# Performance work log

Measured on AMD Instinct MI355X. Metric: run time of the kernel, lower is better.

The kernel has to match this reference:

```python
import jax, jax.numpy as jnp
import numpy as np

IN_CH = 512
HID_CH = 512
NUM_HEADS = HID_CH // 32  # 16 heads, 32 channels each
GN_GROUPS = 32
EPS = 1e-6


def group_norm(x, scale, bias):
    # x: (b, c, t); GroupNorm over (channels-in-group, t)
    b, c, t = x.shape
    xg = x.reshape(b, GN_GROUPS, c // GN_GROUPS, t)
    mean = xg.mean(axis=(2, 3), keepdims=True)
    var = xg.var(axis=(2, 3), keepdims=True)
    xg = (xg - mean) * jax.lax.rsqrt(var + EPS)
    return xg.reshape(b, c, t) * scale[None, :, None] + bias[None, :, None]


def setup_inputs() -> dict:
    key = jax.random.key(0)
    ks = jax.random.split(key, 12)
    b, t = 16, 8192
    s = 0.02
    return {
        "x": jax.random.normal(ks[0], (b, IN_CH, t), dtype=jnp.float32),
        "gn_scale": jnp.ones((IN_CH,), jnp.float32),
        "gn_bias": jnp.zeros((IN_CH,), jnp.float32),
        "wq": jax.random.normal(ks[1], (HID_CH, IN_CH), jnp.float32) * s,
        "bq": jnp.zeros((HID_CH,), jnp.float32),
        "wk": jax.random.normal(ks[2], (HID_CH, IN_CH), jnp.float32) * s,
        "bk": jnp.zeros((HID_CH,), jnp.float32),
        "wv": jax.random.normal(ks[3], (HID_CH, IN_CH), jnp.float32) * s,
        "bv": jnp.zeros((HID_CH,), jnp.float32),
        "wp": jax.random.normal(ks[4], (IN_CH, HID_CH), jnp.float32) * s,
        "bp": jnp.zeros((IN_CH,), jnp.float32),
    }


def reference(x, gn_scale, gn_bias, wq, bq, wk, bk, wv, bv, wp, bp):
    b, _, t = x.shape
    n = NUM_HEADS
    hc = HID_CH // n  # 32 channels per head
    h = group_norm(x, gn_scale, gn_bias)
    # 1x1 conv == channel GEMM: (b,c_in,t) -> (b,c_out,t)
    q = jnp.einsum('oc,bct->bot', wq, h) + bq[None, :, None]
    k = jnp.einsum('oc,bct->bot', wk, h) + bk[None, :, None]
    v = jnp.einsum('oc,bct->bot', wv, h) + bv[None, :, None]
    q = q.reshape(b, n, hc, t)
    k = k.reshape(b, n, hc, t)
    v = v.reshape(b, n, hc, t)
    # q: softmax over channel dim; k: rearranged to (.., t, c), softmax over c
    q = jax.nn.softmax(q, axis=2)          # (b,n,c,t), softmax over c
    k = jax.nn.softmax(k, axis=2)          # softmax over c (dim=-1 after b n t c rearrange)
    w = jnp.einsum('bnct,bndt->bncd', q, k)   # (b,n,c,c) small cxc matrix
    h = jnp.einsum('bncd,bndt->bnct', w, v)   # (b,n,c,t)
    h = h.reshape(b, HID_CH, t)
    out = jnp.einsum('oc,bct->bot', wp, h) + bp[None, :, None]
    return x + out
```

## Files before the change

### kernel.cpp

```cpp
#include <hip/hip_runtime.h>

typedef _Float16 f16;
typedef _Float16 f16x8 __attribute__((ext_vector_type(8)));
typedef _Float16 f16x4 __attribute__((ext_vector_type(4)));
typedef float f32x4 __attribute__((ext_vector_type(4)));
typedef float f32x16 __attribute__((ext_vector_type(16)));


__device__ __forceinline__ void gl_lds16(const f16* g, const void* lds) {
    __builtin_amdgcn_global_load_lds((const __attribute__((address_space(1))) void*)g,
                                     (__attribute__((address_space(3))) void*)lds, 16, 0, 0);
}

__global__ __launch_bounds__(256) void k_tr(const float* __restrict__ x, f16* __restrict__ xT,
                                            float* __restrict__ part,
                                            const float* __restrict__ wv, f16* __restrict__ WvT) {
    int tid = threadIdx.x;
    if (blockIdx.x >= 16384) {
        int idx = (blockIdx.x - 16384) * 256 + tid;
        int c = idx >> 9, e = idx & 511;
        WvT[idx] = (f16)wv[(size_t)e * 512 + c];
        return;
    }
    __shared__ f16 ldsT[64][72];
    int tt = blockIdx.x & 127, ct = (blockIdx.x >> 7) & 7, b = blockIdx.x >> 10;
    int cc = tid >> 2, tq = tid & 3;
    int c = ct * 64 + cc;
    const float* xp = x + ((size_t)b * 512 + c) * 8192 + tt * 64 + tq * 16;
    float s = 0.f, s2 = 0.f;
#pragma unroll
    for (int q4 = 0; q4 < 4; ++q4) {
        f32x4 v = *(const f32x4*)(xp + q4 * 4);
#pragma unroll
        for (int j = 0; j < 4; ++j) {
            ldsT[tq * 16 + q4 * 4 + j][cc] = (f16)v[j];
            s += v[j]; s2 += v[j] * v[j];
        }
    }
#pragma unroll
    for (int k = 1; k < 64; k <<= 1) { s += __shfl_xor(s, k); s2 += __shfl_xor(s2, k); }
    if ((tid & 63) == 0) {
        float* pp = part + (((size_t)b * 32 + ct * 4 + (tid >> 6)) * 128 + tt) * 2;
        pp[0] = s; pp[1] = s2;
    }
    __syncthreads();
    int tl = tid >> 2, cq = tid & 3;
    f16x8 v0 = *(const f16x8*)(&ldsT[tl][cq * 16]);
    f16x8 v1 = *(const f16x8*)(&ldsT[tl][cq * 16 + 8]);
    f16* hp = xT + ((size_t)b * 8192 + tt * 64 + tl) * 512 + ct * 64 + cq * 16;
    *(f16x8*)(hp) = v0;
    *(f16x8*)(hp + 8) = v1;
}

__global__ __launch_bounds__(256) void k_prep(const float* __restrict__ wq, const float* __restrict__ wk,
                                              const float* __restrict__ wv,
                                              const float* __restrict__ gsc, const float* __restrict__ gbi,
                                              const float* __restrict__ part,
                                              const float* __restrict__ bq, const float* __restrict__ bk,
                                              f16* __restrict__ Wqkp2, float* __restrict__ qkb,
                                              float* __restrict__ u, float* __restrict__ stats) {
    __shared__ float scn[512], bi[512], red[256];
    int tid = threadIdx.x;
    int blk = blockIdx.x;
    int b = (blk < 256) ? (blk >> 4) : ((blk - 256) >> 3);
    {
        int g = tid >> 3, ch = tid & 7;
        const float* pp = part + (((size_t)b * 32 + g) * 128 + ch * 16) * 2;
        float s = 0.f, s2 = 0.f;
        for (int t2 = 0; t2 < 16; ++t2) { s += pp[t2 * 2]; s2 += pp[t2 * 2 + 1]; }
        scn[tid] = s; bi[tid] = s2;
    }
    __syncthreads();
    if (tid < 32) {
        float S = 0.f, S2 = 0.f;
#pragma unroll
        for (int j = 0; j < 8; ++j) { S += scn[tid * 8 + j]; S2 += bi[tid * 8 + j]; }
        float mean = S * (1.f / 131072.f);
        float var  = S2 * (1.f / 131072.f) - mean * mean;
        float rstd = rsqrtf(var + 1e-6f);
        red[tid] = mean;
        red[128 + tid] = rstd;
        if (blk >= 256 && ((blk - 256) & 7) == 0) {
            stats[(b * 32 + tid) * 2 + 0] = mean;
            stats[(b * 32 + tid) * 2 + 1] = rstd;
        }
    }
    __syncthreads();
    for (int i = tid; i < 512; i += 256) {
        float sc = gsc[i] * red[128 + (i >> 4)];
        scn[i] = sc;
        bi[i] = gbi[i] - red[i >> 4] * sc;
    }
    __syncthreads();
    if (blk < 256) {
        int rg = blk & 15;
        int pr = rg * 64 + (tid >> 2);
        int cq = tid & 3;
        int hg = pr >> 8, ri = pr & 255;
        int hl = ri >> 6, qk = (ri >> 5) & 1, ch = ri & 31;
        int src = (hg * 4 + hl) * 32 + ch;
        const float* wrow = (qk ? wk : wq) + (size_t)src * 512;
        f16* orow = Wqkp2 + ((size_t)b * 1024 + pr) * 512;
        float dot = 0.f;
        for (int c0 = cq * 128; c0 < cq * 128 + 128; c0 += 8) {
            f16x8 o8;
#pragma unroll
            for (int j = 0; j < 8; ++j) {
                float wv_ = wrow[c0 + j] * scn[c0 + j];
                o8[j] = (f16)wv_;
                dot += wv_ * bi[c0 + j];
            }
            *(f16x8*)(orow + c0) = o8;
        }
        red[tid] = dot;
        __syncthreads();
        if (cq == 0)
            qkb[(size_t)b * 1024 + pr] = red[tid] + red[tid + 1] + red[tid + 2] + red[tid + 3]
                                         + (qk ? bk[src] : bq[src]);
    } else {
        int ug = (blk - 256) & 7;
        int e = ug * 64 + (tid >> 2);
        int cq = tid & 3;
        const float* wrow = wv + (size_t)e * 512;
        float dot = 0.f;
        for (int c = cq * 128; c < cq * 128 + 128; ++c) dot += wrow[c] * bi[c];
        red[tid] = dot;
        __syncthreads();
        if (cq == 0) u[(size_t)b * 512 + e] = red[tid] + red[tid + 1] + red[tid + 2] + red[tid + 3];
    }
}

__device__ __forceinline__ void gemm_core(const f16* __restrict__ Abase, int lda,
                                          const f16* __restrict__ Bbase,
                                          char* smem, int tid, f32x4 acc[4][4]) {
    const int lane = tid & 63, wave = tid >> 6;
    const int wm = wave >> 1, wn = wave & 1;
    char* As = smem;
    char* Bs = smem + 16384;
    const int srow = (lane >> 3);
    const int schunk = (lane & 7) ^ srow;
    for (int kt = 0; kt < 8; ++kt) {
#pragma unroll
        for (int i = 0; i < 4; ++i) {
            int row = (wave * 4 + i) * 8 + srow;
            gl_lds16(Abase + (size_t)row * lda + kt * 64 + schunk * 8, As + (wave * 4 + i) * 1024);
            gl_lds16(Bbase + (size_t)row * 512 + kt * 64 + schunk * 8, Bs + (wave * 4 + i) * 1024);
        }
        __syncthreads();
#pragma unroll
        for (int ks = 0; ks < 2; ++ks) {
            f16x8 af[4], bf[4];
#pragma unroll
            for (int i = 0; i < 4; ++i) {
                int row = wm * 64 + i * 16 + (lane & 15);
                int ch = (ks * 4 + (lane >> 4)) ^ (lane & 7);
                af[i] = *(const f16x8*)(As + row * 128 + ch * 16);
            }
#pragma unroll
            for (int j = 0; j < 4; ++j) {
                int row = wn * 64 + j * 16 + (lane & 15);
                int ch = (ks * 4 + (lane >> 4)) ^ (lane & 7);
                bf[j] = *(const f16x8*)(Bs + row * 128 + ch * 16);
            }
#pragma unroll
            for (int i = 0; i < 4; ++i)
#pragma unroll
                for (int j = 0; j < 4; ++j)
                    acc[i][j] = __builtin_amdgcn_mfma_f32_16x16x32_f16(af[i], bf[j], acc[i][j], 0, 0, 0);
        }
        __syncthreads();
    }
}

__global__ __launch_bounds__(256, 2) void k_qk_w(const f16* __restrict__ xT, const f16* __restrict__ Wqkp2,
                                                 const float* __restrict__ qkb, f16* __restrict__ w_part) {
    __shared__ __align__(16) char smem[49152];
    int tid = threadIdx.x, lane = tid & 63, wave = tid >> 6;
    int bid = blockIdx.x;
    int lb = (bid & 7) * 512 + (bid >> 3);
    int batch = lb >> 8;
    int rem = lb & 255;
    int tt = rem >> 2, hg = rem & 3;
    const f16* Abase = Wqkp2 + ((size_t)batch * 1024 + hg * 256) * 512;
    const f16* Bbase = xT + ((size_t)batch * 8192 + (size_t)tt * 128) * 512;
    char* As = smem;
    char* Bs = smem + 32768;
    const int srow = lane >> 3;
    const int schunk = (lane & 7) ^ srow;
    f32x4 acc[4][8];
#pragma unroll
    for (int i = 0; i < 4; ++i)
#pragma unroll
        for (int j = 0; j < 8; ++j) acc[i][j] = (f32x4){0.f, 0.f, 0.f, 0.f};

    for (int kt = 0; kt < 8; ++kt) {
#pragma unroll
        for (int i = 0; i < 8; ++i) {
            int g = wave * 8 + i;
            gl_lds16(Abase + (size_t)(g * 8 + srow) * 512 + kt * 64 + schunk * 8, As + g * 1024);
        }
#pragma unroll
        for (int i = 0; i < 4; ++i) {
            int g = wave * 4 + i;
            gl_lds16(Bbase + (size_t)(g * 8 + srow) * 512 + kt * 64 + schunk * 8, Bs + g * 1024);
        }
        __syncthreads();
#pragma unroll
        for (int ks = 0; ks < 2; ++ks) {
            f16x8 af[4];
#pragma unroll
            for (int i = 0; i < 4; ++i) {
                int row = wave * 64 + i * 16 + (lane & 15);
                int ch = (ks * 4 + (lane >> 4)) ^ (lane & 7);
                af[i] = *(const f16x8*)(As + row * 128 + ch * 16);
            }
#pragma unroll
            for (int j = 0; j < 8; ++j) {
                int row = j * 16 + (lane & 15);
                int ch = (ks * 4 + (lane >> 4)) ^ (lane & 7);
                f16x8 bf = *(const f16x8*)(Bs + row * 128 + ch * 16);
#pragma unroll
                for (int i = 0; i < 4; ++i)
                    acc[i][j] = __builtin_amdgcn_mfma_f32_16x16x32_f16(af[i], bf, acc[i][j], 0, 0, 0);
            }
        }
        __syncthreads();
    }

    float qb[2][8];
#pragma unroll
    for (int qk = 0; qk < 2; ++qk)
#pragma unroll
        for (int i2 = 0; i2 < 2; ++i2)
#pragma unroll
            for (int r = 0; r < 4; ++r)
                qb[qk][i2 * 4 + r] = qkb[(size_t)batch * 1024 + hg * 256 + wave * 64 + qk * 32 +
                                         i2 * 16 + (lane >> 4) * 4 + r];
    f16* qbuf = (f16*)(smem + wave * 9216);
    f16* kbuf = qbuf + 32 * 72;
    f32x16 wacc;
#pragma unroll
    for (int i = 0; i < 16; ++i) wacc[i] = 0.f;

#pragma unroll
    for (int th = 0; th < 2; ++th) {
#pragma unroll
        for (int jl = 0; jl < 4; ++jl) {
            int j = th * 4 + jl;
#pragma unroll
            for (int qk = 0; qk < 2; ++qk) {
                int ib = qk * 2;
                float v0[8];
#pragma unroll
                for (int i2 = 0; i2 < 2; ++i2)
#pragma unroll
                    for (int r = 0; r < 4; ++r)
                        v0[i2 * 4 + r] = acc[ib + i2][j][r] + qb[qk][i2 * 4 + r];
                float mx = v0[0];
#pragma unroll
                for (int i = 1; i < 8; ++i) mx = fmaxf(mx, v0[i]);
                mx = fmaxf(mx, __shfl_xor(mx, 16));
                mx = fmaxf(mx, __shfl_xor(mx, 32));
                float s = 0.f;
#pragma unroll
                for (int i = 0; i < 8; ++i) { v0[i] = __expf(v0[i] - mx); s += v0[i]; }
                s += __shfl_xor(s, 16);
                s += __shfl_xor(s, 32);
                float inv = 1.f / s;
                f16* dst = qk ? kbuf : qbuf;
                int tcol = jl * 16 + (lane & 15);
#pragma unroll
                for (int i2 = 0; i2 < 2; ++i2)
#pragma unroll
                    for (int r = 0; r < 4; ++r) {
                        int c = i2 * 16 + (lane >> 4) * 4 + r;
                        dst[c * 72 + tcol] = (f16)(v0[i2 * 4 + r] * inv);
                    }
            }
        }
#pragma unroll
        for (int ks = 0; ks < 4; ++ks) {
            f16x8 a  = *(const f16x8*)(qbuf + (lane & 31) * 72 + ks * 16 + (lane >> 5) * 8);
            f16x8 bb = *(const f16x8*)(kbuf + (lane & 31) * 72 + ks * 16 + (lane >> 5) * 8);
            wacc = __builtin_amdgcn_mfma_f32_32x32x16_f16(a, bb, wacc, 0, 0, 0);
        }
    }
    int ghead = hg * 4 + wave;
    f16* wpo = w_part + (((size_t)tt * 16 + batch) * 16 + ghead) * 1024;
#pragma unroll
    for (int r = 0; r < 16; ++r) {
        int row = (r & 3) + 8 * (r >> 2) + 4 * (lane >> 5);
        wpo[row * 32 + (lane & 31)] = (f16)wacc[r];
    }
}

__global__ __launch_bounds__(256) void k_wreduce(const f16* __restrict__ w_part, float* __restrict__ w_red) {
    int blk = blockIdx.x;
    int tid = threadIdx.x;
    f32x4 s = (f32x4){0.f, 0.f, 0.f, 0.f};
    for (int tt = 0; tt < 64; ++tt) {
        f16x4 v = *(const f16x4*)(w_part + ((size_t)tt * 256 + blk) * 1024 + tid * 4);
#pragma unroll
        for (int j = 0; j < 4; ++j) s[j] += (float)v[j];
    }
    *(f32x4*)(w_red + (size_t)blk * 1024 + tid * 4) = s;
}

__global__ __launch_bounds__(256) void k_wpe(const float* __restrict__ w_red, const float* __restrict__ wp,
                                             const float* __restrict__ bv, const float* __restrict__ u,
                                             const float* __restrict__ bp,
                                             f16* __restrict__ wpe, float* __restrict__ bias_p) {
    __shared__ float wl[16384];
    __shared__ float bred[256];
    int tid = threadIdx.x;
    int b = blockIdx.x >> 3, ot = blockIdx.x & 7;
    for (int idx = tid; idx < 16384; idx += 256) wl[idx] = w_red[(size_t)b * 16384 + idx];
    __syncthreads();
    int o = ot * 64 + (tid >> 2);
    int cq = tid & 3;
    float bacc = 0.f;
#pragma unroll
    for (int ng = 0; ng < 4; ++ng) {
        int n = cq * 4 + ng;
        float a[32];
#pragma unroll
        for (int d = 0; d < 32; ++d) a[d] = 0.f;
        for (int e = 0; e < 32; ++e) {
            float wv = wp[(size_t)o * 512 + n * 32 + e];
#pragma unroll
            for (int d = 0; d < 32; ++d) a[d] += wv * wl[n * 1024 + e * 32 + d];
        }
#pragma unroll
        for (int dc = 0; dc < 4; ++dc) {
            f16x8 o8;
#pragma unroll
            for (int j = 0; j < 8; ++j) o8[j] = (f16)a[dc * 8 + j];
            *(f16x8*)(wpe + ((size_t)b * 512 + o) * 512 + n * 32 + dc * 8) = o8;
        }
#pragma unroll
        for (int d = 0; d < 32; ++d) bacc += a[d] * (bv[n * 32 + d] + u[(size_t)b * 512 + n * 32 + d]);
    }
    bred[tid] = bacc;
    __syncthreads();
    if ((tid & 3) == 0)
        bias_p[(size_t)b * 512 + o] = bp[o] + bred[tid] + bred[tid + 1] + bred[tid + 2] + bred[tid + 3];
}

__global__ __launch_bounds__(256) void k_wfin(const f16* __restrict__ wpe, const f16* __restrict__ WvT,
                                              const float* __restrict__ gsc, const float* __restrict__ stats,
                                              f16* __restrict__ Wfin) {
    __shared__ __align__(16) char smem[34816];
    int tid = threadIdx.x, lane = tid & 63, wave = tid >> 6;
    int wm = wave >> 1, wn = wave & 1;
    int bid = blockIdx.x;
    int b = bid >> 4, mt = (bid >> 2) & 3, nt = bid & 3;
    const f16* Abase = wpe + (size_t)b * 262144 + (size_t)mt * 128 * 512;
    const f16* Bbase = WvT + (size_t)nt * 128 * 512;
    f32x4 acc[4][4];
#pragma unroll
    for (int i = 0; i < 4; ++i)
#pragma unroll
        for (int j = 0; j < 4; ++j) acc[i][j] = (f32x4){0.f, 0.f, 0.f, 0.f};
    gemm_core(Abase, 512, Bbase, smem, tid, acc);
    float scnj[4];
#pragma unroll
    for (int j = 0; j < 4; ++j) {
        int col = nt * 128 + wn * 64 + j * 16 + (lane & 15);
        scnj[j] = gsc[col] * stats[(b * 32 + (col >> 4)) * 2 + 1];
    }
    f16* epi = (f16*)smem;
#pragma unroll
    for (int i = 0; i < 4; ++i)
#pragma unroll
        for (int j = 0; j < 4; ++j)
#pragma unroll
            for (int r = 0; r < 4; ++r) {
                int m = wm * 64 + i * 16 + (lane >> 4) * 4 + r;
                int n = wn * 64 + j * 16 + (lane & 15);
                epi[m * 136 + n] = (f16)(acc[i][j][r] * scnj[j]);
            }
    __syncthreads();
#pragma unroll
    for (int rr = 0; rr < 8; ++rr) {
        int row = wave * 32 + (lane >> 4) * 8 + rr;
        f16x8 vv = *(const f16x8*)(epi + row * 136 + (lane & 15) * 8);
        *(f16x8*)(Wfin + (size_t)b * 262144 + (size_t)(mt * 128 + row) * 512 + nt * 128 + (lane & 15) * 8) = vv;
    }
}

__global__ __launch_bounds__(256, 2) void k_out(const f16* __restrict__ xT, const f16* __restrict__ Wfin,
                                                const float* __restrict__ x, const float* __restrict__ bias_p,
                                                float* __restrict__ out) {
    __shared__ __align__(16) char smem[49152];
    int tid = threadIdx.x, lane = tid & 63, wave = tid >> 6;
    int bid = blockIdx.x;
    int lb = (bid & 7) * 256 + (bid >> 3);
    int batch = lb >> 7;
    int rem = lb & 127;
    int tt = rem >> 1, ot2 = rem & 1;
    const f16* Abase = Wfin + (size_t)batch * 262144 + (size_t)ot2 * 256 * 512;
    const f16* Bbase = xT + ((size_t)batch * 8192 + (size_t)tt * 128) * 512;
    char* As = smem;
    char* Bs = smem + 32768;
    const int srow = lane >> 3;
    const int schunk = (lane & 7) ^ srow;
    f32x4 acc[4][8];
#pragma unroll
    for (int i = 0; i < 4; ++i)
#pragma unroll
        for (int j = 0; j < 8; ++j) acc[i][j] = (f32x4){0.f, 0.f, 0.f, 0.f};

    for (int kt = 0; kt < 8; ++kt) {
#pragma unroll
        for (int i = 0; i < 8; ++i) {
            int g = wave * 8 + i;
            gl_lds16(Abase + (size_t)(g * 8 + srow) * 512 + kt * 64 + schunk * 8, As + g * 1024);
        }
#pragma unroll
        for (int i = 0; i < 4; ++i) {
            int g = wave * 4 + i;
            gl_lds16(Bbase + (size_t)(g * 8 + srow) * 512 + kt * 64 + schunk * 8, Bs + g * 1024);
        }
        __syncthreads();
#pragma unroll
        for (int ks = 0; ks < 2; ++ks) {
            f16x8 af[4];
#pragma unroll
            for (int i = 0; i < 4; ++i) {
                int row = wave * 64 + i * 16 + (lane & 15);
                int ch = (ks * 4 + (lane >> 4)) ^ (lane & 7);
                af[i] = *(const f16x8*)(As + row * 128 + ch * 16);
            }
#pragma unroll
            for (int j = 0; j < 8; ++j) {
                int row = j * 16 + (lane & 15);
                int ch = (ks * 4 + (lane >> 4)) ^ (lane & 7);
                f16x8 bf = *(const f16x8*)(Bs + row * 128 + ch * 16);
#pragma unroll
                for (int i = 0; i < 4; ++i)
                    acc[i][j] = __builtin_amdgcn_mfma_f32_16x16x32_f16(af[i], bf, acc[i][j], 0, 0, 0);
            }
        }
        __syncthreads();
    }

    f16* ep = (f16*)smem;
    const int orow_in = (lane >> 4) * 4;
    for (int pp = 0; pp < 2; ++pp) {
        __syncthreads();
        if ((wave >> 1) == pp) {
            f16* myep = ep + (size_t)(wave & 1) * 64 * 132;
#pragma unroll
            for (int i = 0; i < 4; ++i)
#pragma unroll
                for (int j = 0; j < 8; ++j)
#pragma unroll
                    for (int r = 0; r < 4; ++r)
                        myep[(i * 16 + orow_in + r) * 132 + j * 16 + (lane & 15)] = (f16)acc[i][j][r];
        }
        __syncthreads();
        int o_g0 = ot2 * 256 + pp * 128;
#pragma unroll
        for (int p = 0; p < 16; ++p) {
            int idx = p * 256 + tid;
            int row = idx >> 5;
            int tq = (idx & 31) * 4;
            int o = o_g0 + row;
            float bpv = bias_p[batch * 512 + o];
            size_t g = ((size_t)batch * 512 + o) * 8192 + (size_t)tt * 128 + tq;
            f32x4 xv = *(const f32x4*)(x + g);
            f16x4 lv = *(const f16x4*)(ep + row * 132 + tq);
            f32x4 ov;
#pragma unroll
            for (int j = 0; j < 4; ++j) ov[j] = xv[j] + bpv + (float)lv[j];
            *(f32x4*)(out + g) = ov;
        }
    }
}

extern "C" void kernel_launch(void* const* d_in, const int* in_sizes, int n_in,
                              void* d_out, int out_size, void* d_ws, size_t ws_size,
                              hipStream_t stream) {
    const float* x   = (const float*)d_in[0];
    const float* gsc = (const float*)d_in[1];
    const float* gbi = (const float*)d_in[2];
    const float* wq  = (const float*)d_in[3];
    const float* bq  = (const float*)d_in[4];
    const float* wk  = (const float*)d_in[5];
    const float* bk  = (const float*)d_in[6];
    const float* wv  = (const float*)d_in[7];
    const float* bv  = (const float*)d_in[8];
    const float* wp  = (const float*)d_in[9];
    const float* bp  = (const float*)d_in[10];
    float* out = (float*)d_out;
    char* ws = (char*)d_ws;

    size_t o_stats = 0;
    size_t o_part  = 4096;
    size_t o_qkb   = o_part + 524288;
    size_t o_u     = o_qkb + 65536;
    size_t o_biasp = o_u + 32768;
    size_t o_wvt   = o_biasp + 32768;
    size_t o_wred  = o_wvt + 524288;
    size_t o_wpe   = o_wred + 1048576;
    size_t o_wfin  = o_wpe + 8388608;
    size_t o_wqkp2 = o_wfin + 8388608;
    size_t o_wpart = o_wqkp2 + 16777216;
    size_t o_xT    = o_wpart + 33554432;
    size_t total   = o_xT + 134217728;
    if (ws_size < total) return;

    float* stats  = (float*)(ws + o_stats);
    float* part   = (float*)(ws + o_part);
    float* qkb    = (float*)(ws + o_qkb);
    float* u      = (float*)(ws + o_u);
    float* bias_p = (float*)(ws + o_biasp);
    f16*   WvT    = (f16*)(ws + o_wvt);
    float* w_red  = (float*)(ws + o_wred);
    f16*   wpe    = (f16*)(ws + o_wpe);
    f16*   Wfin   = (f16*)(ws + o_wfin);
    f16*   Wqkp2  = (f16*)(ws + o_wqkp2);
    f16*   w_part = (f16*)(ws + o_wpart);
    f16*   xT     = (f16*)(ws + o_xT);

    k_tr     <<<17408, 256, 0, stream>>>(x, xT, part, wv, WvT);
    k_prep   <<<384,   256, 0, stream>>>(wq, wk, wv, gsc, gbi, part, bq, bk, Wqkp2, qkb, u, stats);
    k_qk_w   <<<4096,  256, 0, stream>>>(xT, Wqkp2, qkb, w_part);
    k_wreduce<<<256,   256, 0, stream>>>(w_part, w_red);
    k_wpe    <<<128,   256, 0, stream>>>(w_red, wp, bv, u, bp, wpe, bias_p);
    k_wfin   <<<256,   256, 0, stream>>>(wpe, WvT, gsc, stats, Wfin);
    k_out    <<<2048,  256, 0, stream>>>(xT, Wfin, x, bias_p, out);
}
```

Measured before the change: 494.2 us.

## Double-buffer k_qk_w GEMM K-loop with async LDS prefetch of next tile

The QK GEMM main loop in k_qk_w now uses 32-wide K tiles in two 24 KB LDS buffers instead of one 64-wide tile per step. The loads for tile kt+1 are issued before the MFMAs on tile kt. A partial vmcnt wait replaces the two full __syncthreads per iteration, and the swizzle is reworked for the narrower 64-byte rows. The aim is to hide global-to-LDS latency behind matrix math. The trade-off is twice as many loop iterations, and there is a data-readiness risk: each wave waits only on its own loads and does not hit a barrier after that wait before reading rows that other waves staged.

```diff
diff --git a/kernel.cpp b/kernel.cpp
--- a/kernel.cpp
+++ b/kernel.cpp
@@ -183,49 +183,55 @@
     int tt = rem >> 2, hg = rem & 3;
     const f16* Abase = Wqkp2 + ((size_t)batch * 1024 + hg * 256) * 512;
     const f16* Bbase = xT + ((size_t)batch * 8192 + (size_t)tt * 128) * 512;
-    char* As = smem;
-    char* Bs = smem + 32768;
-    const int srow = lane >> 3;
-    const int schunk = (lane & 7) ^ srow;
+    const int rowb4 = tid >> 2;
+    const int sc4 = (tid & 3) ^ ((tid >> 3) & 3);
+    const int chR = ((lane >> 4) ^ (((lane & 15) >> 1) & 3)) << 4;
+    const int arow0 = wave * 64 + (lane & 15);
+    const int brow0 = lane & 15;
+
+#define STAGE32(kt1_, buf_)                                                                      \
+    do {                                                                                         \
+        _Pragma("unroll")                                                                        \
+        for (int i_ = 0; i_ < 4; ++i_)                                                           \
+            gl_lds16(Abase + (size_t)(i_ * 64 + rowb4) * 512 + (kt1_) * 32 + sc4 * 8,            \
+                     (buf_) + i_ * 4096 + wave * 1024);                                          \
+        _Pragma("unroll")                                                                        \
+        for (int i_ = 0; i_ < 2; ++i_)                                                           \
+            gl_lds16(Bbase + (size_t)(i_ * 64 + rowb4) * 512 + (kt1_) * 32 + sc4 * 8,            \
+                     (buf_) + 16384 + i_ * 4096 + wave * 1024);                                  \
+    } while (0)
+
     f32x4 acc[4][8];
 #pragma unroll
     for (int i = 0; i < 4; ++i)
 #pragma unroll
         for (int j = 0; j < 8; ++j) acc[i][j] = (f32x4){0.f, 0.f, 0.f, 0.f};
 
-    for (int kt = 0; kt < 8; ++kt) {
-#pragma unroll
-        for (int i = 0; i < 8; ++i) {
-            int g = wave * 8 + i;
-            gl_lds16(Abase + (size_t)(g * 8 + srow) * 512 + kt * 64 + schunk * 8, As + g * 1024);
-        }
-#pragma unroll
-        for (int i = 0; i < 4; ++i) {
-            int g = wave * 4 + i;
-            gl_lds16(Bbase + (size_t)(g * 8 + srow) * 512 + kt * 64 + schunk * 8, Bs + g * 1024);
-        }
-        __syncthreads();
-#pragma unroll
-        for (int ks = 0; ks < 2; ++ks) {
-            f16x8 af[4];
-#pragma unroll
-            for (int i = 0; i < 4; ++i) {
-                int row = wave * 64 + i * 16 + (lane & 15);
-                int ch = (ks * 4 + (lane >> 4)) ^ (lane & 7);
-                af[i] = *(const f16x8*)(As + row * 128 + ch * 16);
-            }
-#pragma unroll
-            for (int j = 0; j < 8; ++j) {
-                int row = j * 16 + (lane & 15);
-                int ch = (ks * 4 + (lane >> 4)) ^ (lane & 7);
-                f16x8 bf = *(const f16x8*)(Bs + row * 128 + ch * 16);
-#pragma unroll
-                for (int i = 0; i < 4; ++i)
-                    acc[i][j] = __builtin_amdgcn_mfma_f32_16x16x32_f16(af[i], bf, acc[i][j], 0, 0, 0);
-            }
-        }
-        __syncthreads();
-    }
+    STAGE32(0, smem);
+    for (int kt = 0; kt < 16; ++kt) {
+        asm volatile("s_barrier" ::: "memory");
+        char* cbuf = smem + (kt & 1) * 24576;
+        char* nbuf = smem + (((kt & 1) ^ 1)) * 24576;
+        if (kt < 15) {
+            STAGE32(kt + 1, nbuf);
+            asm volatile("s_waitcnt vmcnt(6)" ::: "memory");
+        } else {
+            asm volatile("s_waitcnt vmcnt(0)" ::: "memory");
+        }
+        f16x8 af[4];
+#pragma unroll
+        for (int i = 0; i < 4; ++i)
+            af[i] = *(const f16x8*)(cbuf + (arow0 + i * 16) * 64 + chR);
+#pragma unroll
+        for (int j = 0; j < 8; ++j) {
+            f16x8 bf = *(const f16x8*)(cbuf + 16384 + (brow0 + j * 16) * 64 + chR);
+#pragma unroll
+            for (int i = 0; i < 4; ++i)
+                acc[i][j] = __builtin_amdgcn_mfma_f32_16x16x32_f16(af[i], bf, acc[i][j], 0, 0, 0);
+        }
+    }
+#undef STAGE32
+    __syncthreads();
 
     float qb[2][8];
 #pragma unroll
```

Result: no change. 497.4 us (+0.6%).
